# Performance work log

Hardware: AMD Instinct MI355X
Metric: run time of the kernel (lower is better)

The kernel has to match this reference:

```python
import jax, jax.numpy as jnp
import numpy as np

B, S, D = 2, 2048, 1024
H = 16
HD = D // H  # 64
SCALE = HD ** -0.5


def setup_inputs() -> dict:
    key = jax.random.key(0)
    ks = jax.random.split(key, 9)
    init = lambda k, shape: jax.random.normal(k, shape, dtype=jnp.float32) * (1.0 / np.sqrt(shape[-1]))
    return {
        "x": jax.random.normal(ks[0], (B, S, D), dtype=jnp.float32),
        "wq": init(ks[1], (D, D)), "bq": jnp.zeros((D,), jnp.float32),
        "wk": init(ks[2], (D, D)), "bk": jnp.zeros((D,), jnp.float32),
        "wv": init(ks[3], (D, D)), "bv": jnp.zeros((D,), jnp.float32),
        "wo": init(ks[4], (D, D)), "bo": jnp.zeros((D,), jnp.float32),
    }


def reference(x, wq, bq, wk, bk, wv, bv, wo, bo):
    b, s, d = x.shape
    # projections -> [b, h, s, hd]
    q = (x @ wq + bq).reshape(b, s, H, HD).transpose(0, 2, 1, 3)
    k = (x @ wk + bk).reshape(b, s, H, HD).transpose(0, 2, 1, 3)
    v = (x @ wv + bv).reshape(b, s, H, HD).transpose(0, 2, 1, 3)
    # full causal attention (chunked loop in original computes exactly this)
    scores = jnp.einsum("bhqd,bhkd->bhqk", q, k) * SCALE
    causal = jnp.tril(jnp.ones((s, s), dtype=bool))
    scores = jnp.where(causal, scores, -jnp.inf)
    weights = jax.nn.softmax(scores, axis=-1)
    out = jnp.einsum("bhqk,bhkd->bhqd", weights, v)
    out = out.transpose(0, 2, 1, 3).reshape(b, s, d)
    return out @ wo + bo
```

## Files before the change

kernel.cpp:

```cpp
#include <hip/hip_runtime.h>
#include <hip/hip_bf16.h>
#include <cstdint>

#define B_  2
#define S_  2048
#define D_  1024
#define H_  16
#define HD_ 64
#define M_  (B_ * S_)
static constexpr float SC_LOG2E = 0.125f * 1.44269504088896f;

typedef __bf16 bf16x8 __attribute__((ext_vector_type(8)));
typedef __bf16 bf16x4 __attribute__((ext_vector_type(4)));
typedef float  f32x4  __attribute__((ext_vector_type(4)));

__device__ __forceinline__ unsigned short f2b(float f) {
  union { float f; unsigned u; } x; x.f = f;
  unsigned r = x.u + 0x7FFF + ((x.u >> 16) & 1);
  return (unsigned short)(r >> 16);
}

__device__ __forceinline__ void gl_lds16(const unsigned short* g, unsigned short* l) {
  __builtin_amdgcn_global_load_lds((const __attribute__((address_space(1))) void*)g,
                                   (__attribute__((address_space(3))) void*)l, 16, 0, 0);
}

__device__ __forceinline__ void bar_lgkm() {
  asm volatile("s_waitcnt lgkmcnt(0)\n\ts_barrier" ::: "memory");
}
__device__ __forceinline__ void bar_vm2() {
  asm volatile("s_waitcnt vmcnt(2) lgkmcnt(0)\n\ts_barrier" ::: "memory");
}
__device__ __forceinline__ void bar_vm0() {
  asm volatile("s_waitcnt vmcnt(0) lgkmcnt(0)\n\ts_barrier" ::: "memory");
}

__global__ void cvt_all_kernel(const float* __restrict__ x,
                               const float* __restrict__ w0, const float* __restrict__ w1,
                               const float* __restrict__ w2, const float* __restrict__ w3,
                               unsigned short* __restrict__ xb,
                               unsigned short* __restrict__ o0, unsigned short* __restrict__ o1,
                               unsigned short* __restrict__ o2, unsigned short* __restrict__ o3) {
  int tx = threadIdx.x, ty = threadIdx.y;
  if (blockIdx.z == 4) {
    int tid = ty * 32 + tx;
    int base = ((int)blockIdx.y * 32 + (int)blockIdx.x) * 1024 + tid;
    const float4* xf = (const float4*)x;
    ushort4* ob = (ushort4*)xb;
#pragma unroll
    for (int j = 0; j < 4; j++) {
      float4 v = xf[base + j * 256];
      ushort4 r;
      r.x = f2b(v.x); r.y = f2b(v.y); r.z = f2b(v.z); r.w = f2b(v.w);
      ob[base + j * 256] = r;
    }
    return;
  }
  const float* w = blockIdx.z == 0 ? w0 : blockIdx.z == 1 ? w1 : blockIdx.z == 2 ? w2 : w3;
  unsigned short* o = blockIdx.z == 0 ? o0 : blockIdx.z == 1 ? o1 : blockIdx.z == 2 ? o2 : o3;
  __shared__ float t[32][33];
  int x0 = blockIdx.x * 32, y0 = blockIdx.y * 32;
#pragma unroll
  for (int j = 0; j < 4; j++)
    t[ty + j * 8][tx] = w[(size_t)(y0 + ty + j * 8) * D_ + x0 + tx];
  __syncthreads();
#pragma unroll
  for (int j = 0; j < 4; j++)
    o[(size_t)(x0 + ty + j * 8) * D_ + y0 + tx] = f2b(t[tx][ty + j * 8]);
}

__global__ __launch_bounds__(512) void qkv_gemm_kernel(
    const unsigned short* __restrict__ xb,
    const unsigned short* __restrict__ wqt, const unsigned short* __restrict__ wkt,
    const unsigned short* __restrict__ wvt,
    const float* __restrict__ bq, const float* __restrict__ bk, const float* __restrict__ bv,
    unsigned short* __restrict__ qo, unsigned short* __restrict__ ko, unsigned short* __restrict__ vo) {
  const unsigned short* wt = blockIdx.z == 0 ? wqt : blockIdx.z == 1 ? wkt : wvt;
  const float* bias        = blockIdx.z == 0 ? bq  : blockIdx.z == 1 ? bk  : bv;
  unsigned short* out      = blockIdx.z == 0 ? qo  : blockIdx.z == 1 ? ko  : vo;
  const float scl = blockIdx.z == 0 ? SC_LOG2E : 1.0f;

  __shared__ __align__(16) unsigned short smem[6 * 4096];
  const int tid = threadIdx.x;
  const int lane = tid & 63, wid = tid >> 6;
  const int wm = wid & 1, wn = wid >> 1;
  const int m0 = blockIdx.x * 128, n0 = blockIdx.y * 128;
  const int l15 = lane & 15, q4 = lane >> 4;
  const int srow = tid >> 2, skc = (tid & 3) * 8;

  f32x4 zero = {0.f, 0.f, 0.f, 0.f};
  f32x4 acc[4][2];
#pragma unroll
  for (int mt = 0; mt < 4; mt++)
#pragma unroll
    for (int nt = 0; nt < 2; nt++) acc[mt][nt] = zero;

  const unsigned short* ap = xb + (size_t)(m0 + srow) * D_ + skc;
  const unsigned short* bp = wt + (size_t)(n0 + srow) * D_ + skc;
  gl_lds16(ap,      smem + tid * 8);
  gl_lds16(bp,      smem + 12288 + tid * 8);
  gl_lds16(ap + 32, smem + 4096 + tid * 8);
  gl_lds16(bp + 32, smem + 12288 + 4096 + tid * 8);

  int bc = 0;
  for (int it = 0; it < 32; it++) {
    if (it < 31) bar_vm2(); else bar_vm0();
    if (it + 2 < 32) {
      int bn_ = bc < 1 ? bc + 2 : bc - 1;
      gl_lds16(ap + (it + 2) * 32, smem + bn_ * 4096 + tid * 8);
      gl_lds16(bp + (it + 2) * 32, smem + 12288 + bn_ * 4096 + tid * 8);
    }
    const unsigned short* Ab = smem + bc * 4096;
    const unsigned short* Bb = smem + 12288 + bc * 4096;
    bf16x8 af[4], bfv[2];
#pragma unroll
    for (int mt = 0; mt < 4; mt++) af[mt]  = *(const bf16x8*)(Ab + (wm * 64 + mt * 16 + l15) * 32 + q4 * 8);
#pragma unroll
    for (int nt = 0; nt < 2; nt++) bfv[nt] = *(const bf16x8*)(Bb + (wn * 32 + nt * 16 + l15) * 32 + q4 * 8);
#pragma unroll
    for (int mt = 0; mt < 4; mt++)
#pragma unroll
      for (int nt = 0; nt < 2; nt++)
        acc[mt][nt] = __builtin_amdgcn_mfma_f32_16x16x32_bf16(af[mt], bfv[nt], acc[mt][nt], 0, 0, 0);
    bc = bc == 2 ? 0 : bc + 1;
  }

  if (blockIdx.z < 2) {
#pragma unroll
    for (int nt = 0; nt < 2; nt++) {
      int n = n0 + wn * 32 + nt * 16 + l15;
      float bn = bias[n];
      int h = n >> 6, hd = n & 63;
#pragma unroll
      for (int mt = 0; mt < 4; mt++) {
#pragma unroll
        for (int r = 0; r < 4; r++) {
          int m = m0 + wm * 64 + mt * 16 + q4 * 4 + r;
          int b = m >> 11, s = m & (S_ - 1);
          out[(((size_t)(b * H_ + h)) * S_ + s) * HD_ + hd] = f2b((acc[mt][nt][r] + bn) * scl);
        }
      }
    }
  } else {
    unsigned short* buf = smem;
#pragma unroll
    for (int p = 0; p < 2; p++) {
      __syncthreads();
      if ((wn >> 1) == p) {
#pragma unroll
        for (int nt = 0; nt < 2; nt++) {
          int np = (wn & 1) * 32 + nt * 16 + l15;
          float bn = bias[n0 + p * 64 + np];
#pragma unroll
          for (int mt = 0; mt < 4; mt++) {
            f32x4 vb = acc[mt][nt];
            vb[0] += bn; vb[1] += bn; vb[2] += bn; vb[3] += bn;
            bf16x4 pk = __builtin_convertvector(vb, bf16x4);
            *(bf16x4*)(&buf[np * 136 + wm * 64 + mt * 16 + q4 * 4]) = pk;
          }
        }
      }
      __syncthreads();
#pragma unroll
      for (int i = 0; i < 2; i++) {
        int ci = tid + i * 512;
        int np = ci >> 4, c = ci & 15;
        int n = n0 + p * 64 + np;
        int h = n >> 6, hd = n & 63;
        int m = m0 + c * 8;
        int b = m >> 11, s = m & (S_ - 1);
        *(uint4*)(out + (((size_t)(b * H_ + h)) * HD_ + hd) * S_ + s) = *(const uint4*)(buf + np * 136 + c * 8);
      }
    }
  }
}

__global__ __launch_bounds__(512, 4) void attn_kernel(
    const unsigned short* __restrict__ Q, const unsigned short* __restrict__ K,
    const unsigned short* __restrict__ Vt_g, unsigned short* __restrict__ O) {
  const int id = blockIdx.x;
  const int u = id >> 8, v = id & 255;
  const int bh = v & 31;
  const int t = v >> 5;
  const int qi = u ? (15 - t) : t;
  const int b = bh >> 4, h = bh & 15;
  const unsigned short* Qh = Q    + (size_t)bh * S_ * HD_;
  const unsigned short* Kh = K    + (size_t)bh * S_ * HD_;
  const unsigned short* Vh = Vt_g + (size_t)bh * HD_ * S_;

  __shared__ __align__(16) unsigned short Ks[2][64 * 64];
  __shared__ __align__(16) unsigned short Vt[2][64 * 64];
  __shared__ __align__(16) unsigned short Ps[8][16 * 72];

  const int tid = threadIdx.x, lane = tid & 63, w = tid >> 6;
  const int l15 = lane & 15, q4 = lane >> 4;
  const int kx = (l15 & 7) << 3;
  const int kcA = (q4 * 8) ^ kx, kcB = (q4 * 8 + 32) ^ kx;
  const int vc0 = (q4 * 8) ^ kx, vc1 = (32 + q4 * 8) ^ kx;
  unsigned short* Pw = &Ps[w][0];

  const int srow = tid >> 3;
  const int scolS = (((tid & 7) ^ (srow & 7)) * 8);
  const unsigned short* kg = Kh + (size_t)srow * HD_ + (tid & 7) * 8;
  const unsigned short* vg = Vh + (size_t)srow * S_  + (tid & 7) * 8;

  const int q0 = qi * 128;
  const int nkt = 2 * qi + 2;
  const int qlo = q0 + w * 16;
  const int qmax = qlo + 15;
  const int qrow = qlo + l15;

  const unsigned short* qp = Qh + (size_t)qrow * HD_ + q4 * 8;
  bf16x8 bq0 = *(const bf16x8*)(qp);
  bf16x8 bq1 = *(const bf16x8*)(qp + 32);

  float m_i = -1e30f, l_i = 0.f;
  f32x4 zero = {0.f, 0.f, 0.f, 0.f};
  f32x4 o_acc[4];
#pragma unroll
  for (int t4 = 0; t4 < 4; t4++) o_acc[t4] = zero;

  uint4 kp = *(const uint4*)(kg);
  uint4 vp = *(const uint4*)(vg);

  for (int kt = 0; kt < nkt; kt++) {
    const int k0 = kt * 64;
    unsigned short* Kb = Ks[kt & 1];
    unsigned short* Vb = Vt[kt & 1];
    *(uint4*)(Kb + srow * 64 + scolS) = kp;
    *(uint4*)(Vb + srow * 64 + scolS) = vp;
    bar_lgkm();
    if (kt + 1 < nkt) {
      kp = *(const uint4*)(kg + (size_t)(kt + 1) * 64 * HD_);
      vp = *(const uint4*)(vg + (kt + 1) * 64);
    }

    if (k0 <= qmax) {
      f32x4 sc[4];
#pragma unroll
      for (int nt = 0; nt < 4; nt++) sc[nt] = zero;
      __builtin_amdgcn_s_setprio(1);
#pragma unroll
      for (int nt = 0; nt < 4; nt++) {
        bf16x8 ak0 = *(const bf16x8*)(Kb + (nt * 16 + l15) * 64 + kcA);
        bf16x8 ak1 = *(const bf16x8*)(Kb + (nt * 16 + l15) * 64 + kcB);
        sc[nt] = __builtin_amdgcn_mfma_f32_16x16x32_bf16(ak0, bq0, sc[nt], 0, 0, 0);
        sc[nt] = __builtin_amdgcn_mfma_f32_16x16x32_bf16(ak1, bq1, sc[nt], 0, 0, 0);
      }
      __builtin_amdgcn_s_setprio(0);

      if ((k0 + 63) > qlo) {
#pragma unroll
        for (int nt = 0; nt < 4; nt++)
#pragma unroll
          for (int r = 0; r < 4; r++) {
            int key = k0 + nt * 16 + q4 * 4 + r;
            if (key > qrow) sc[nt][r] = -1e30f;
          }
      }

      float am[4];
#pragma unroll
      for (int nt = 0; nt < 4; nt++)
        am[nt] = fmaxf(fmaxf(sc[nt][0], sc[nt][1]), fmaxf(sc[nt][2], sc[nt][3]));
      am[0] = fmaxf(am[0], am[2]); am[1] = fmaxf(am[1], am[3]);
      float mx = fmaxf(am[0], am[1]);
      mx = fmaxf(mx, __shfl_xor(mx, 16));
      mx = fmaxf(mx, __shfl_xor(mx, 32));
      mx = fmaxf(mx, m_i);

      if (!__all(mx - m_i <= 10.0f)) {
        float alpha = __builtin_amdgcn_exp2f(m_i - mx);
        m_i = mx;
        l_i *= alpha;
#pragma unroll
        for (int r = 0; r < 4; r++) {
          float ar = __shfl(alpha, q4 * 4 + r);
          o_acc[0][r] *= ar; o_acc[1][r] *= ar; o_acc[2][r] *= ar; o_acc[3][r] *= ar;
        }
      }

      float sm[4];
#pragma unroll
      for (int nt = 0; nt < 4; nt++) {
        f32x4 pv;
#pragma unroll
        for (int r = 0; r < 4; r++) pv[r] = __builtin_amdgcn_exp2f(sc[nt][r] - m_i);
        sc[nt] = pv;
        sm[nt] = (pv[0] + pv[1]) + (pv[2] + pv[3]);
      }
      float rs = (sm[0] + sm[2]) + (sm[1] + sm[3]);
      rs += __shfl_xor(rs, 16);
      rs += __shfl_xor(rs, 32);
      l_i += rs;

#pragma unroll
      for (int nt = 0; nt < 4; nt++) {
        bf16x4 pk = __builtin_convertvector(sc[nt], bf16x4);
        *(bf16x4*)(Pw + l15 * 72 + nt * 16 + q4 * 4) = pk;
      }
      __threadfence_block();
      bf16x8 ap0 = *(const bf16x8*)(Pw + l15 * 72 + q4 * 8);
      bf16x8 ap1 = *(const bf16x8*)(Pw + l15 * 72 + 32 + q4 * 8);
      __builtin_amdgcn_s_setprio(1);
#pragma unroll
      for (int nt2 = 0; nt2 < 4; nt2++) {
        bf16x8 bv0 = *(const bf16x8*)(Vb + (nt2 * 16 + l15) * 64 + vc0);
        o_acc[nt2] = __builtin_amdgcn_mfma_f32_16x16x32_bf16(ap0, bv0, o_acc[nt2], 0, 0, 0);
      }
#pragma unroll
      for (int nt2 = 0; nt2 < 4; nt2++) {
        bf16x8 bv1 = *(const bf16x8*)(Vb + (nt2 * 16 + l15) * 64 + vc1);
        o_acc[nt2] = __builtin_amdgcn_mfma_f32_16x16x32_bf16(ap1, bv1, o_acc[nt2], 0, 0, 0);
      }
      __builtin_amdgcn_s_setprio(0);
    }
  }

#pragma unroll
  for (int r = 0; r < 4; r++) {
    float lr = __shfl(l_i, q4 * 4 + r);
    float inv = 1.0f / lr;
    int s_ = q0 + w * 16 + q4 * 4 + r;
#pragma unroll
    for (int nt2 = 0; nt2 < 4; nt2++)
      O[((size_t)(b * S_ + s_)) * D_ + h * HD_ + nt2 * 16 + l15] = f2b(o_acc[nt2][r] * inv);
  }
}

__global__ __launch_bounds__(512) void out_gemm_kernel(
    const unsigned short* __restrict__ ab, const unsigned short* __restrict__ wot,
    const float* __restrict__ bo, float* __restrict__ out) {
  __shared__ __align__(16) unsigned short smem[6 * 4096];
  const int tid = threadIdx.x;
  const int lane = tid & 63, wid = tid >> 6;
  const int wm = wid & 1, wn = wid >> 1;
  const int m0 = blockIdx.x * 128, n0 = blockIdx.y * 128;
  const int l15 = lane & 15, q4 = lane >> 4;
  const int srow = tid >> 2, skc = (tid & 3) * 8;

  f32x4 zero = {0.f, 0.f, 0.f, 0.f};
  f32x4 acc[4][2];
#pragma unroll
  for (int mt = 0; mt < 4; mt++)
#pragma unroll
    for (int nt = 0; nt < 2; nt++) acc[mt][nt] = zero;

  const unsigned short* ap = ab  + (size_t)(m0 + srow) * D_ + skc;
  const unsigned short* bp = wot + (size_t)(n0 + srow) * D_ + skc;
  gl_lds16(ap,      smem + tid * 8);
  gl_lds16(bp,      smem + 12288 + tid * 8);
  gl_lds16(ap + 32, smem + 4096 + tid * 8);
  gl_lds16(bp + 32, smem + 12288 + 4096 + tid * 8);

  int bc = 0;
  for (int it = 0; it < 32; it++) {
    if (it < 31) bar_vm2(); else bar_vm0();
    if (it + 2 < 32) {
      int bn_ = bc < 1 ? bc + 2 : bc - 1;
      gl_lds16(ap + (it + 2) * 32, smem + bn_ * 4096 + tid * 8);
      gl_lds16(bp + (it + 2) * 32, smem + 12288 + bn_ * 4096 + tid * 8);
    }
    const unsigned short* Ab = smem + bc * 4096;
    const unsigned short* Bb = smem + 12288 + bc * 4096;
    bf16x8 af[4], bfv[2];
#pragma unroll
    for (int mt = 0; mt < 4; mt++) af[mt]  = *(const bf16x8*)(Ab + (wm * 64 + mt * 16 + l15) * 32 + q4 * 8);
#pragma unroll
    for (int nt = 0; nt < 2; nt++) bfv[nt] = *(const bf16x8*)(Bb + (wn * 32 + nt * 16 + l15) * 32 + q4 * 8);
#pragma unroll
    for (int mt = 0; mt < 4; mt++)
#pragma unroll
      for (int nt = 0; nt < 2; nt++)
        acc[mt][nt] = __builtin_amdgcn_mfma_f32_16x16x32_bf16(af[mt], bfv[nt], acc[mt][nt], 0, 0, 0);
    bc = bc == 2 ? 0 : bc + 1;
  }

#pragma unroll
  for (int nt = 0; nt < 2; nt++) {
    int n = n0 + wn * 32 + nt * 16 + l15;
    float bn = bo[n];
#pragma unroll
    for (int mt = 0; mt < 4; mt++) {
#pragma unroll
      for (int r = 0; r < 4; r++) {
        int m = m0 + wm * 64 + mt * 16 + q4 * 4 + r;
        out[(size_t)m * D_ + n] = acc[mt][nt][r] + bn;
      }
    }
  }
}

extern "C" void kernel_launch(void* const* d_in, const int* in_sizes, int n_in,
                              void* d_out, int out_size, void* d_ws, size_t ws_size,
                              hipStream_t stream) {
  const float* x  = (const float*)d_in[0];
  const float* wq = (const float*)d_in[1];
  const float* bq = (const float*)d_in[2];
  const float* wk = (const float*)d_in[3];
  const float* bk = (const float*)d_in[4];
  const float* wv = (const float*)d_in[5];
  const float* bv = (const float*)d_in[6];
  const float* wo = (const float*)d_in[7];
  const float* bo = (const float*)d_in[8];
  float* out = (float*)d_out;

  char* ws = (char*)d_ws;
  unsigned short* xb  = (unsigned short*)(ws);
  unsigned short* wqt = (unsigned short*)(ws + (8u  << 20));
  unsigned short* wkt = (unsigned short*)(ws + (10u << 20));
  unsigned short* wvt = (unsigned short*)(ws + (12u << 20));
  unsigned short* wot = (unsigned short*)(ws + (14u << 20));
  unsigned short* qb  = (unsigned short*)(ws + (16u << 20));
  unsigned short* kb  = (unsigned short*)(ws + (24u << 20));
  unsigned short* vtg = (unsigned short*)(ws + (32u << 20));
  unsigned short* ab  = xb;

  cvt_all_kernel<<<dim3(32, 32, 5), dim3(32, 8), 0, stream>>>(x, wq, wk, wv, wo, xb, wqt, wkt, wvt, wot);
  qkv_gemm_kernel<<<dim3(32, 8, 3), dim3(512), 0, stream>>>(xb, wqt, wkt, wvt, bq, bk, bv, qb, kb, vtg);
  attn_kernel<<<dim3(512), dim3(512), 0, stream>>>(qb, kb, vtg, ab);
  out_gemm_kernel<<<dim3(32, 8), dim3(512), 0, stream>>>(ab, wot, bo, out);
}
```

Measured before the change: 181.7 us.

## Restructure attention onto 32x32x16 MFMA with register P and direct-to-LDS loads

The attention kernel now runs 4 waves per block, each owning 32 query rows, and uses 32x32x16 bf16 MFMAs in place of 16x16x32. The P matrix is packed to bf16 with v_cvt_pk and rearranged with permlane32_swap, so it stays in registers instead of going through LDS. K and V tiles are loaded with global_load_lds double buffering instead of register staging, and the output is staged through LDS so the global stores are coalesced 16-byte writes. The goal is to cut LDS traffic and instruction overhead per MFMA. In exchange the kernel holds larger accumulator vectors, which may raise register pressure and lower occupancy.

```diff
diff --git a/kernel.cpp b/kernel.cpp
--- a/kernel.cpp
+++ b/kernel.cpp
@@ -13,11 +13,22 @@
 typedef __bf16 bf16x8 __attribute__((ext_vector_type(8)));
 typedef __bf16 bf16x4 __attribute__((ext_vector_type(4)));
 typedef float  f32x4  __attribute__((ext_vector_type(4)));
+typedef float  f32x16 __attribute__((ext_vector_type(16)));
+typedef unsigned u32x2 __attribute__((ext_vector_type(2)));
 
 __device__ __forceinline__ unsigned short f2b(float f) {
   union { float f; unsigned u; } x; x.f = f;
   unsigned r = x.u + 0x7FFF + ((x.u >> 16) & 1);
   return (unsigned short)(r >> 16);
+}
+
+__device__ __forceinline__ unsigned cvtpk(float lo, float hi) {
+  unsigned r;
+  asm("v_cvt_pk_bf16_f32 %0, %1, %2" : "=v"(r) : "v"(lo), "v"(hi));
+  return r;
+}
+__device__ __forceinline__ u32x2 pswap(unsigned a, unsigned b) {
+  return __builtin_amdgcn_permlane32_swap(a, b, false, false);
 }
 
 __device__ __forceinline__ void gl_lds16(const unsigned short* g, unsigned short* l) {
@@ -175,14 +186,13 @@
   }
 }
 
-__global__ __launch_bounds__(512, 4) void attn_kernel(
+__global__ __launch_bounds__(256, 2) void attn_kernel(
     const unsigned short* __restrict__ Q, const unsigned short* __restrict__ K,
     const unsigned short* __restrict__ Vt_g, unsigned short* __restrict__ O) {
   const int id = blockIdx.x;
-  const int u = id >> 8, v = id & 255;
-  const int bh = v & 31;
-  const int t = v >> 5;
-  const int qi = u ? (15 - t) : t;
+  const int bh = id & 31;
+  const int t = id >> 5;
+  const int qi = (t < 8) ? (15 - t) : (t - 8);
   const int b = bh >> 4, h = bh & 15;
   const unsigned short* Qh = Q    + (size_t)bh * S_ * HD_;
   const unsigned short* Kh = K    + (size_t)bh * S_ * HD_;
@@ -190,141 +200,159 @@
 
   __shared__ __align__(16) unsigned short Ks[2][64 * 64];
   __shared__ __align__(16) unsigned short Vt[2][64 * 64];
-  __shared__ __align__(16) unsigned short Ps[8][16 * 72];
+  __shared__ __align__(16) unsigned short Sw[4][32 * 72];
 
   const int tid = threadIdx.x, lane = tid & 63, w = tid >> 6;
-  const int l15 = lane & 15, q4 = lane >> 4;
-  const int kx = (l15 & 7) << 3;
-  const int kcA = (q4 * 8) ^ kx, kcB = (q4 * 8 + 32) ^ kx;
-  const int vc0 = (q4 * 8) ^ kx, vc1 = (32 + q4 * 8) ^ kx;
-  unsigned short* Pw = &Ps[w][0];
-
-  const int srow = tid >> 3;
-  const int scolS = (((tid & 7) ^ (srow & 7)) * 8);
-  const unsigned short* kg = Kh + (size_t)srow * HD_ + (tid & 7) * 8;
-  const unsigned short* vg = Vh + (size_t)srow * S_  + (tid & 7) * 8;
-
-  const int q0 = qi * 128;
-  const int nkt = 2 * qi + 2;
-  const int qlo = q0 + w * 16;
-  const int qmax = qlo + 15;
-  const int qrow = qlo + l15;
-
-  const unsigned short* qp = Qh + (size_t)qrow * HD_ + q4 * 8;
-  bf16x8 bq0 = *(const bf16x8*)(qp);
-  bf16x8 bq1 = *(const bf16x8*)(qp + 32);
+  const int myk = lane & 31, hi5 = lane >> 5;
+  const int q0 = qi * 128, nkt = 2 * qi + 2;
+  const int qlo = q0 + w * 32, qmax = qlo + 31;
+  const int qrow = qlo + myk;
+
+  int kso[2], vso[2];
+#pragma unroll
+  for (int j = 0; j < 2; j++) {
+    int c = tid + j * 256, row = c >> 3, c8 = c & 7;
+    int sc_ = (c8 ^ (row & 7)) * 8;
+    kso[j] = row * HD_ + sc_;
+    vso[j] = row * S_ + sc_;
+  }
+
+  bf16x8 qf[4];
+#pragma unroll
+  for (int kk = 0; kk < 4; kk++)
+    qf[kk] = *(const bf16x8*)(Qh + (size_t)qrow * HD_ + kk * 16 + hi5 * 8);
+
+#pragma unroll
+  for (int j = 0; j < 2; j++) {
+    gl_lds16(Kh + kso[j], &Ks[0][0] + (tid + j * 256) * 8);
+    gl_lds16(Vh + vso[j], &Vt[0][0] + (tid + j * 256) * 8);
+  }
 
   float m_i = -1e30f, l_i = 0.f;
-  f32x4 zero = {0.f, 0.f, 0.f, 0.f};
-  f32x4 o_acc[4];
-#pragma unroll
-  for (int t4 = 0; t4 < 4; t4++) o_acc[t4] = zero;
-
-  uint4 kp = *(const uint4*)(kg);
-  uint4 vp = *(const uint4*)(vg);
+  f32x16 oa0, oa1;
+#pragma unroll
+  for (int i = 0; i < 16; i++) { oa0[i] = 0.f; oa1[i] = 0.f; }
 
   for (int kt = 0; kt < nkt; kt++) {
     const int k0 = kt * 64;
-    unsigned short* Kb = Ks[kt & 1];
-    unsigned short* Vb = Vt[kt & 1];
-    *(uint4*)(Kb + srow * 64 + scolS) = kp;
-    *(uint4*)(Vb + srow * 64 + scolS) = vp;
-    bar_lgkm();
+    bar_vm0();
     if (kt + 1 < nkt) {
-      kp = *(const uint4*)(kg + (size_t)(kt + 1) * 64 * HD_);
-      vp = *(const uint4*)(vg + (kt + 1) * 64);
-    }
-
-    if (k0 <= qmax) {
-      f32x4 sc[4];
-#pragma unroll
-      for (int nt = 0; nt < 4; nt++) sc[nt] = zero;
-      __builtin_amdgcn_s_setprio(1);
-#pragma unroll
-      for (int nt = 0; nt < 4; nt++) {
-        bf16x8 ak0 = *(const bf16x8*)(Kb + (nt * 16 + l15) * 64 + kcA);
-        bf16x8 ak1 = *(const bf16x8*)(Kb + (nt * 16 + l15) * 64 + kcB);
-        sc[nt] = __builtin_amdgcn_mfma_f32_16x16x32_bf16(ak0, bq0, sc[nt], 0, 0, 0);
-        sc[nt] = __builtin_amdgcn_mfma_f32_16x16x32_bf16(ak1, bq1, sc[nt], 0, 0, 0);
-      }
-      __builtin_amdgcn_s_setprio(0);
-
-      if ((k0 + 63) > qlo) {
-#pragma unroll
-        for (int nt = 0; nt < 4; nt++)
-#pragma unroll
-          for (int r = 0; r < 4; r++) {
-            int key = k0 + nt * 16 + q4 * 4 + r;
-            if (key > qrow) sc[nt][r] = -1e30f;
-          }
-      }
-
-      float am[4];
-#pragma unroll
-      for (int nt = 0; nt < 4; nt++)
-        am[nt] = fmaxf(fmaxf(sc[nt][0], sc[nt][1]), fmaxf(sc[nt][2], sc[nt][3]));
-      am[0] = fmaxf(am[0], am[2]); am[1] = fmaxf(am[1], am[3]);
-      float mx = fmaxf(am[0], am[1]);
-      mx = fmaxf(mx, __shfl_xor(mx, 16));
-      mx = fmaxf(mx, __shfl_xor(mx, 32));
-      mx = fmaxf(mx, m_i);
-
-      if (!__all(mx - m_i <= 10.0f)) {
-        float alpha = __builtin_amdgcn_exp2f(m_i - mx);
-        m_i = mx;
-        l_i *= alpha;
-#pragma unroll
-        for (int r = 0; r < 4; r++) {
-          float ar = __shfl(alpha, q4 * 4 + r);
-          o_acc[0][r] *= ar; o_acc[1][r] *= ar; o_acc[2][r] *= ar; o_acc[3][r] *= ar;
-        }
-      }
-
-      float sm[4];
-#pragma unroll
-      for (int nt = 0; nt < 4; nt++) {
-        f32x4 pv;
-#pragma unroll
-        for (int r = 0; r < 4; r++) pv[r] = __builtin_amdgcn_exp2f(sc[nt][r] - m_i);
-        sc[nt] = pv;
-        sm[nt] = (pv[0] + pv[1]) + (pv[2] + pv[3]);
-      }
-      float rs = (sm[0] + sm[2]) + (sm[1] + sm[3]);
-      rs += __shfl_xor(rs, 16);
-      rs += __shfl_xor(rs, 32);
-      l_i += rs;
-
-#pragma unroll
-      for (int nt = 0; nt < 4; nt++) {
-        bf16x4 pk = __builtin_convertvector(sc[nt], bf16x4);
-        *(bf16x4*)(Pw + l15 * 72 + nt * 16 + q4 * 4) = pk;
-      }
-      __threadfence_block();
-      bf16x8 ap0 = *(const bf16x8*)(Pw + l15 * 72 + q4 * 8);
-      bf16x8 ap1 = *(const bf16x8*)(Pw + l15 * 72 + 32 + q4 * 8);
-      __builtin_amdgcn_s_setprio(1);
-#pragma unroll
-      for (int nt2 = 0; nt2 < 4; nt2++) {
-        bf16x8 bv0 = *(const bf16x8*)(Vb + (nt2 * 16 + l15) * 64 + vc0);
-        o_acc[nt2] = __builtin_amdgcn_mfma_f32_16x16x32_bf16(ap0, bv0, o_acc[nt2], 0, 0, 0);
-      }
-#pragma unroll
-      for (int nt2 = 0; nt2 < 4; nt2++) {
-        bf16x8 bv1 = *(const bf16x8*)(Vb + (nt2 * 16 + l15) * 64 + vc1);
-        o_acc[nt2] = __builtin_amdgcn_mfma_f32_16x16x32_bf16(ap1, bv1, o_acc[nt2], 0, 0, 0);
-      }
-      __builtin_amdgcn_s_setprio(0);
-    }
-  }
-
-#pragma unroll
-  for (int r = 0; r < 4; r++) {
-    float lr = __shfl(l_i, q4 * 4 + r);
-    float inv = 1.0f / lr;
-    int s_ = q0 + w * 16 + q4 * 4 + r;
-#pragma unroll
-    for (int nt2 = 0; nt2 < 4; nt2++)
-      O[((size_t)(b * S_ + s_)) * D_ + h * HD_ + nt2 * 16 + l15] = f2b(o_acc[nt2][r] * inv);
+      unsigned short* Kd = &Ks[(kt + 1) & 1][0];
+      unsigned short* Vd = &Vt[(kt + 1) & 1][0];
+#pragma unroll
+      for (int j = 0; j < 2; j++) {
+        gl_lds16(Kh + (kt + 1) * 64 * HD_ + kso[j], Kd + (tid + j * 256) * 8);
+        gl_lds16(Vh + (kt + 1) * 64 + vso[j],       Vd + (tid + j * 256) * 8);
+      }
+    }
+    if (k0 > qmax) continue;
+
+    const unsigned short* Kb = &Ks[kt & 1][0];
+    const unsigned short* Vb = &Vt[kt & 1][0];
+
+    f32x16 sc0, sc1;
+#pragma unroll
+    for (int i = 0; i < 16; i++) { sc0[i] = 0.f; sc1[i] = 0.f; }
+    __builtin_amdgcn_s_setprio(1);
+#pragma unroll
+    for (int kk = 0; kk < 4; kk++) {
+      const int off = ((kk * 2 + hi5) ^ (myk & 7)) * 8;
+      bf16x8 a0 = *(const bf16x8*)(Kb + myk * 64 + off);
+      bf16x8 a1 = *(const bf16x8*)(Kb + (32 + myk) * 64 + off);
+      sc0 = __builtin_amdgcn_mfma_f32_32x32x16_bf16(a0, qf[kk], sc0, 0, 0, 0);
+      sc1 = __builtin_amdgcn_mfma_f32_32x32x16_bf16(a1, qf[kk], sc1, 0, 0, 0);
+    }
+    __builtin_amdgcn_s_setprio(0);
+
+    if (k0 + 63 > qlo) {
+#pragma unroll
+      for (int rg = 0; rg < 16; rg++) {
+        const int r = (rg & 3) + 8 * (rg >> 2) + 4 * hi5;
+        if (k0 + r > qrow)      sc0[rg] = -1e30f;
+        if (k0 + 32 + r > qrow) sc1[rg] = -1e30f;
+      }
+    }
+
+    float am[8];
+#pragma unroll
+    for (int i = 0; i < 8; i++)
+      am[i] = fmaxf(fmaxf(sc0[i], sc0[i + 8]), fmaxf(sc1[i], sc1[i + 8]));
+#pragma unroll
+    for (int sr = 4; sr > 0; sr >>= 1)
+#pragma unroll
+      for (int i = 0; i < sr; i++) am[i] = fmaxf(am[i], am[i + sr]);
+    float mx = fmaxf(am[0], __shfl_xor(am[0], 32));
+    mx = fmaxf(mx, m_i);
+
+    if (!__all(mx - m_i <= 10.0f)) {
+      float alpha = __builtin_amdgcn_exp2f(m_i - mx);
+      m_i = mx;
+      l_i *= alpha;
+#pragma unroll
+      for (int i = 0; i < 16; i++) { oa0[i] *= alpha; oa1[i] *= alpha; }
+    }
+
+#pragma unroll
+    for (int i = 0; i < 16; i++) sc0[i] = __builtin_amdgcn_exp2f(sc0[i] - m_i);
+#pragma unroll
+    for (int i = 0; i < 16; i++) sc1[i] = __builtin_amdgcn_exp2f(sc1[i] - m_i);
+    float sm[8];
+#pragma unroll
+    for (int i = 0; i < 8; i++) sm[i] = (sc0[i] + sc0[i + 8]) + (sc1[i] + sc1[i + 8]);
+#pragma unroll
+    for (int sr = 4; sr > 0; sr >>= 1)
+#pragma unroll
+      for (int i = 0; i < sr; i++) sm[i] += sm[i + sr];
+    l_i += sm[0] + __shfl_xor(sm[0], 32);
+
+    unsigned wa[8], wb[8];
+#pragma unroll
+    for (int i = 0; i < 8; i++) {
+      wa[i] = cvtpk(sc0[2 * i], sc0[2 * i + 1]);
+      wb[i] = cvtpk(sc1[2 * i], sc1[2 * i + 1]);
+    }
+    union { unsigned u[4]; bf16x8 v; } pf0, pf1, pf2, pf3;
+    { u32x2 s0 = pswap(wa[0], wa[2]), s1 = pswap(wa[1], wa[3]);
+      pf0.u[0] = s0[0]; pf0.u[1] = s1[0]; pf0.u[2] = s0[1]; pf0.u[3] = s1[1]; }
+    { u32x2 s0 = pswap(wa[4], wa[6]), s1 = pswap(wa[5], wa[7]);
+      pf1.u[0] = s0[0]; pf1.u[1] = s1[0]; pf1.u[2] = s0[1]; pf1.u[3] = s1[1]; }
+    { u32x2 s0 = pswap(wb[0], wb[2]), s1 = pswap(wb[1], wb[3]);
+      pf2.u[0] = s0[0]; pf2.u[1] = s1[0]; pf2.u[2] = s0[1]; pf2.u[3] = s1[1]; }
+    { u32x2 s0 = pswap(wb[4], wb[6]), s1 = pswap(wb[5], wb[7]);
+      pf3.u[0] = s0[0]; pf3.u[1] = s1[0]; pf3.u[2] = s0[1]; pf3.u[3] = s1[1]; }
+
+    __builtin_amdgcn_s_setprio(1);
+#pragma unroll
+    for (int ks = 0; ks < 4; ks++) {
+      const int off = ((ks * 2 + hi5) ^ (myk & 7)) * 8;
+      bf16x8 v0 = *(const bf16x8*)(Vb + myk * 64 + off);
+      bf16x8 v1 = *(const bf16x8*)(Vb + (32 + myk) * 64 + off);
+      bf16x8 pk = ks == 0 ? pf0.v : ks == 1 ? pf1.v : ks == 2 ? pf2.v : pf3.v;
+      oa0 = __builtin_amdgcn_mfma_f32_32x32x16_bf16(v0, pk, oa0, 0, 0, 0);
+      oa1 = __builtin_amdgcn_mfma_f32_32x32x16_bf16(v1, pk, oa1, 0, 0, 0);
+    }
+    __builtin_amdgcn_s_setprio(0);
+  }
+
+  const float inv = 1.0f / l_i;
+#pragma unroll
+  for (int i = 0; i < 16; i++) { oa0[i] *= inv; oa1[i] *= inv; }
+  unsigned short* sw = &Sw[w][0];
+#pragma unroll
+  for (int g = 0; g < 4; g++) {
+    u32x2 d0, d1;
+    d0[0] = cvtpk(oa0[4 * g], oa0[4 * g + 1]);
+    d0[1] = cvtpk(oa0[4 * g + 2], oa0[4 * g + 3]);
+    d1[0] = cvtpk(oa1[4 * g], oa1[4 * g + 1]);
+    d1[1] = cvtpk(oa1[4 * g + 2], oa1[4 * g + 3]);
+    *(u32x2*)(sw + myk * 72 + g * 8 + 4 * hi5)      = d0;
+    *(u32x2*)(sw + myk * 72 + 32 + g * 8 + 4 * hi5) = d1;
+  }
+#pragma unroll
+  for (int rr = 0; rr < 4; rr++) {
+    int qq = rr * 8 + (lane >> 3);
+    uint4 d = *(const uint4*)(sw + qq * 72 + (lane & 7) * 8);
+    *(uint4*)(O + ((size_t)(b * S_ + qlo + qq)) * D_ + h * 64 + (lane & 7) * 8) = d;
   }
 }
 
@@ -418,6 +446,6 @@
 
   cvt_all_kernel<<<dim3(32, 32, 5), dim3(32, 8), 0, stream>>>(x, wq, wk, wv, wo, xb, wqt, wkt, wvt, wot);
   qkv_gemm_kernel<<<dim3(32, 8, 3), dim3(512), 0, stream>>>(xb, wqt, wkt, wvt, bq, bk, bv, qb, kb, vtg);
-  attn_kernel<<<dim3(512), dim3(512), 0, stream>>>(qb, kb, vtg, ab);
+  attn_kernel<<<dim3(512), dim3(256), 0, stream>>>(qb, kb, vtg, ab);
   out_gemm_kernel<<<dim3(32, 8), dim3(512), 0, stream>>>(ab, wot, bo, out);
 }
```

Measured after the change: 188.1 us. 1.03x slower.

## Drop LDS staging of K/V in attention and shrink query tiles to 64 rows

Applied to the files above, without the earlier changes.

The attention kernel now reads K and V fragments straight from global memory (relying on L1/L2) instead of double-buffering them through shared memory with a barrier each iteration. Blocks shrink to 256 threads covering 64 query rows, and the grid doubles to 1024 with a four-way reversed tile ordering to balance causal work. This removes the per-tile barriers and LDS traffic and raises block count, but it trades that for redundant global/cache loads, since each wave fetches K/V independently with less coalesced access.

```diff
diff --git a/kernel.cpp b/kernel.cpp
--- a/kernel.cpp
+++ b/kernel.cpp
@@ -175,39 +175,28 @@
   }
 }
 
-__global__ __launch_bounds__(512, 4) void attn_kernel(
+__global__ __launch_bounds__(256, 4) void attn_kernel(
     const unsigned short* __restrict__ Q, const unsigned short* __restrict__ K,
     const unsigned short* __restrict__ Vt_g, unsigned short* __restrict__ O) {
   const int id = blockIdx.x;
-  const int u = id >> 8, v = id & 255;
-  const int bh = v & 31;
-  const int t = v >> 5;
-  const int qi = u ? (15 - t) : t;
+  const int bh = id & 31;
+  const int tIdx = id >> 5;
+  const int u = tIdx >> 3, t8 = tIdx & 7;
+  const int qi = (u == 0) ? t8 : (u == 1) ? (15 - t8) : (u == 2) ? (16 + t8) : (31 - t8);
   const int b = bh >> 4, h = bh & 15;
   const unsigned short* Qh = Q    + (size_t)bh * S_ * HD_;
   const unsigned short* Kh = K    + (size_t)bh * S_ * HD_;
   const unsigned short* Vh = Vt_g + (size_t)bh * HD_ * S_;
 
-  __shared__ __align__(16) unsigned short Ks[2][64 * 64];
-  __shared__ __align__(16) unsigned short Vt[2][64 * 64];
-  __shared__ __align__(16) unsigned short Ps[8][16 * 72];
+  __shared__ __align__(16) unsigned short Ps[4][16 * 72];
 
   const int tid = threadIdx.x, lane = tid & 63, w = tid >> 6;
   const int l15 = lane & 15, q4 = lane >> 4;
-  const int kx = (l15 & 7) << 3;
-  const int kcA = (q4 * 8) ^ kx, kcB = (q4 * 8 + 32) ^ kx;
-  const int vc0 = (q4 * 8) ^ kx, vc1 = (32 + q4 * 8) ^ kx;
   unsigned short* Pw = &Ps[w][0];
 
-  const int srow = tid >> 3;
-  const int scolS = (((tid & 7) ^ (srow & 7)) * 8);
-  const unsigned short* kg = Kh + (size_t)srow * HD_ + (tid & 7) * 8;
-  const unsigned short* vg = Vh + (size_t)srow * S_  + (tid & 7) * 8;
-
-  const int q0 = qi * 128;
-  const int nkt = 2 * qi + 2;
+  const int q0 = qi * 64;
+  const int nkt = qi + 1;
   const int qlo = q0 + w * 16;
-  const int qmax = qlo + 15;
   const int qrow = qlo + l15;
 
   const unsigned short* qp = Qh + (size_t)qrow * HD_ + q4 * 8;
@@ -220,101 +209,88 @@
 #pragma unroll
   for (int t4 = 0; t4 < 4; t4++) o_acc[t4] = zero;
 
-  uint4 kp = *(const uint4*)(kg);
-  uint4 vp = *(const uint4*)(vg);
-
   for (int kt = 0; kt < nkt; kt++) {
     const int k0 = kt * 64;
-    unsigned short* Kb = Ks[kt & 1];
-    unsigned short* Vb = Vt[kt & 1];
-    *(uint4*)(Kb + srow * 64 + scolS) = kp;
-    *(uint4*)(Vb + srow * 64 + scolS) = vp;
-    bar_lgkm();
-    if (kt + 1 < nkt) {
-      kp = *(const uint4*)(kg + (size_t)(kt + 1) * 64 * HD_);
-      vp = *(const uint4*)(vg + (kt + 1) * 64);
-    }
-
-    if (k0 <= qmax) {
-      f32x4 sc[4];
-#pragma unroll
-      for (int nt = 0; nt < 4; nt++) sc[nt] = zero;
-      __builtin_amdgcn_s_setprio(1);
-#pragma unroll
-      for (int nt = 0; nt < 4; nt++) {
-        bf16x8 ak0 = *(const bf16x8*)(Kb + (nt * 16 + l15) * 64 + kcA);
-        bf16x8 ak1 = *(const bf16x8*)(Kb + (nt * 16 + l15) * 64 + kcB);
-        sc[nt] = __builtin_amdgcn_mfma_f32_16x16x32_bf16(ak0, bq0, sc[nt], 0, 0, 0);
-        sc[nt] = __builtin_amdgcn_mfma_f32_16x16x32_bf16(ak1, bq1, sc[nt], 0, 0, 0);
-      }
-      __builtin_amdgcn_s_setprio(0);
-
-      if ((k0 + 63) > qlo) {
-#pragma unroll
-        for (int nt = 0; nt < 4; nt++)
-#pragma unroll
-          for (int r = 0; r < 4; r++) {
-            int key = k0 + nt * 16 + q4 * 4 + r;
-            if (key > qrow) sc[nt][r] = -1e30f;
-          }
-      }
-
-      float am[4];
+
+    f32x4 sc[4];
+#pragma unroll
+    for (int nt = 0; nt < 4; nt++) sc[nt] = zero;
+    __builtin_amdgcn_s_setprio(1);
+#pragma unroll
+    for (int nt = 0; nt < 4; nt++) {
+      const unsigned short* kr = Kh + (size_t)(k0 + nt * 16 + l15) * HD_ + q4 * 8;
+      bf16x8 ak0 = *(const bf16x8*)(kr);
+      bf16x8 ak1 = *(const bf16x8*)(kr + 32);
+      sc[nt] = __builtin_amdgcn_mfma_f32_16x16x32_bf16(ak0, bq0, sc[nt], 0, 0, 0);
+      sc[nt] = __builtin_amdgcn_mfma_f32_16x16x32_bf16(ak1, bq1, sc[nt], 0, 0, 0);
+    }
+    __builtin_amdgcn_s_setprio(0);
+
+    if (k0 + 63 > qlo) {
 #pragma unroll
       for (int nt = 0; nt < 4; nt++)
-        am[nt] = fmaxf(fmaxf(sc[nt][0], sc[nt][1]), fmaxf(sc[nt][2], sc[nt][3]));
-      am[0] = fmaxf(am[0], am[2]); am[1] = fmaxf(am[1], am[3]);
-      float mx = fmaxf(am[0], am[1]);
-      mx = fmaxf(mx, __shfl_xor(mx, 16));
-      mx = fmaxf(mx, __shfl_xor(mx, 32));
-      mx = fmaxf(mx, m_i);
-
-      if (!__all(mx - m_i <= 10.0f)) {
-        float alpha = __builtin_amdgcn_exp2f(m_i - mx);
-        m_i = mx;
-        l_i *= alpha;
 #pragma unroll
         for (int r = 0; r < 4; r++) {
-          float ar = __shfl(alpha, q4 * 4 + r);
-          o_acc[0][r] *= ar; o_acc[1][r] *= ar; o_acc[2][r] *= ar; o_acc[3][r] *= ar;
+          int key = k0 + nt * 16 + q4 * 4 + r;
+          if (key > qrow) sc[nt][r] = -1e30f;
         }
-      }
-
-      float sm[4];
-#pragma unroll
-      for (int nt = 0; nt < 4; nt++) {
-        f32x4 pv;
-#pragma unroll
-        for (int r = 0; r < 4; r++) pv[r] = __builtin_amdgcn_exp2f(sc[nt][r] - m_i);
-        sc[nt] = pv;
-        sm[nt] = (pv[0] + pv[1]) + (pv[2] + pv[3]);
-      }
-      float rs = (sm[0] + sm[2]) + (sm[1] + sm[3]);
-      rs += __shfl_xor(rs, 16);
-      rs += __shfl_xor(rs, 32);
-      l_i += rs;
-
-#pragma unroll
-      for (int nt = 0; nt < 4; nt++) {
-        bf16x4 pk = __builtin_convertvector(sc[nt], bf16x4);
-        *(bf16x4*)(Pw + l15 * 72 + nt * 16 + q4 * 4) = pk;
-      }
-      __threadfence_block();
-      bf16x8 ap0 = *(const bf16x8*)(Pw + l15 * 72 + q4 * 8);
-      bf16x8 ap1 = *(const bf16x8*)(Pw + l15 * 72 + 32 + q4 * 8);
-      __builtin_amdgcn_s_setprio(1);
-#pragma unroll
-      for (int nt2 = 0; nt2 < 4; nt2++) {
-        bf16x8 bv0 = *(const bf16x8*)(Vb + (nt2 * 16 + l15) * 64 + vc0);
-        o_acc[nt2] = __builtin_amdgcn_mfma_f32_16x16x32_bf16(ap0, bv0, o_acc[nt2], 0, 0, 0);
-      }
-#pragma unroll
-      for (int nt2 = 0; nt2 < 4; nt2++) {
-        bf16x8 bv1 = *(const bf16x8*)(Vb + (nt2 * 16 + l15) * 64 + vc1);
-        o_acc[nt2] = __builtin_amdgcn_mfma_f32_16x16x32_bf16(ap1, bv1, o_acc[nt2], 0, 0, 0);
-      }
-      __builtin_amdgcn_s_setprio(0);
-    }
+    }
+
+    float am[4];
+#pragma unroll
+    for (int nt = 0; nt < 4; nt++)
+      am[nt] = fmaxf(fmaxf(sc[nt][0], sc[nt][1]), fmaxf(sc[nt][2], sc[nt][3]));
+    am[0] = fmaxf(am[0], am[2]); am[1] = fmaxf(am[1], am[3]);
+    float mx = fmaxf(am[0], am[1]);
+    mx = fmaxf(mx, __shfl_xor(mx, 16));
+    mx = fmaxf(mx, __shfl_xor(mx, 32));
+    mx = fmaxf(mx, m_i);
+
+    if (!__all(mx - m_i <= 10.0f)) {
+      float alpha = __builtin_amdgcn_exp2f(m_i - mx);
+      m_i = mx;
+      l_i *= alpha;
+#pragma unroll
+      for (int r = 0; r < 4; r++) {
+        float ar = __shfl(alpha, q4 * 4 + r);
+        o_acc[0][r] *= ar; o_acc[1][r] *= ar; o_acc[2][r] *= ar; o_acc[3][r] *= ar;
+      }
+    }
+
+    float sm[4];
+#pragma unroll
+    for (int nt = 0; nt < 4; nt++) {
+      f32x4 pv;
+#pragma unroll
+      for (int r = 0; r < 4; r++) pv[r] = __builtin_amdgcn_exp2f(sc[nt][r] - m_i);
+      sc[nt] = pv;
+      sm[nt] = (pv[0] + pv[1]) + (pv[2] + pv[3]);
+    }
+    float rs = (sm[0] + sm[2]) + (sm[1] + sm[3]);
+    rs += __shfl_xor(rs, 16);
+    rs += __shfl_xor(rs, 32);
+    l_i += rs;
+
+#pragma unroll
+    for (int nt = 0; nt < 4; nt++) {
+      bf16x4 pk = __builtin_convertvector(sc[nt], bf16x4);
+      *(bf16x4*)(Pw + l15 * 72 + nt * 16 + q4 * 4) = pk;
+    }
+    __threadfence_block();
+    bf16x8 ap0 = *(const bf16x8*)(Pw + l15 * 72 + q4 * 8);
+    bf16x8 ap1 = *(const bf16x8*)(Pw + l15 * 72 + 32 + q4 * 8);
+    __builtin_amdgcn_s_setprio(1);
+#pragma unroll
+    for (int nt2 = 0; nt2 < 4; nt2++) {
+      bf16x8 bv0 = *(const bf16x8*)(Vh + (size_t)(nt2 * 16 + l15) * S_ + k0 + q4 * 8);
+      o_acc[nt2] = __builtin_amdgcn_mfma_f32_16x16x32_bf16(ap0, bv0, o_acc[nt2], 0, 0, 0);
+    }
+#pragma unroll
+    for (int nt2 = 0; nt2 < 4; nt2++) {
+      bf16x8 bv1 = *(const bf16x8*)(Vh + (size_t)(nt2 * 16 + l15) * S_ + k0 + 32 + q4 * 8);
+      o_acc[nt2] = __builtin_amdgcn_mfma_f32_16x16x32_bf16(ap1, bv1, o_acc[nt2], 0, 0, 0);
+    }
+    __builtin_amdgcn_s_setprio(0);
   }
 
 #pragma unroll
@@ -418,6 +394,6 @@
 
   cvt_all_kernel<<<dim3(32, 32, 5), dim3(32, 8), 0, stream>>>(x, wq, wk, wv, wo, xb, wqt, wkt, wvt, wot);
   qkv_gemm_kernel<<<dim3(32, 8, 3), dim3(512), 0, stream>>>(xb, wqt, wkt, wvt, bq, bk, bv, qb, kb, vtg);
-  attn_kernel<<<dim3(512), dim3(512), 0, stream>>>(qb, kb, vtg, ab);
+  attn_kernel<<<dim3(1024), dim3(256), 0, stream>>>(qb, kb, vtg, ab);
   out_gemm_kernel<<<dim3(32, 8), dim3(512), 0, stream>>>(ab, wot, bo, out);
 }
```

Result: slower. 261.0 us (+43.6%).

## Load V fragments directly from global into registers, drop V LDS staging

Applied to the files above, without the earlier changes.

The attention kernel stops staging V^T tiles through shared memory. Each wave now loads its V MFMA operands straight from global memory per active key tile. This removes the V LDS stores and reads and halves LDS use, which may raise occupancy. In exchange every wave redundantly fetches the same V tile and global latency lands directly before the PV MFMAs with no software prefetch. The block-to-query-tile mapping also changes so that heavy (late) query tiles are dispatched first.

```diff
diff --git a/kernel.cpp b/kernel.cpp
--- a/kernel.cpp
+++ b/kernel.cpp
@@ -179,30 +179,26 @@
     const unsigned short* __restrict__ Q, const unsigned short* __restrict__ K,
     const unsigned short* __restrict__ Vt_g, unsigned short* __restrict__ O) {
   const int id = blockIdx.x;
-  const int u = id >> 8, v = id & 255;
-  const int bh = v & 31;
-  const int t = v >> 5;
-  const int qi = u ? (15 - t) : t;
+  const int bh = id & 31;
+  const int t = id >> 5;
+  const int qi = (t < 8) ? (15 - t) : (t - 8);
   const int b = bh >> 4, h = bh & 15;
   const unsigned short* Qh = Q    + (size_t)bh * S_ * HD_;
   const unsigned short* Kh = K    + (size_t)bh * S_ * HD_;
   const unsigned short* Vh = Vt_g + (size_t)bh * HD_ * S_;
 
   __shared__ __align__(16) unsigned short Ks[2][64 * 64];
-  __shared__ __align__(16) unsigned short Vt[2][64 * 64];
   __shared__ __align__(16) unsigned short Ps[8][16 * 72];
 
   const int tid = threadIdx.x, lane = tid & 63, w = tid >> 6;
   const int l15 = lane & 15, q4 = lane >> 4;
   const int kx = (l15 & 7) << 3;
   const int kcA = (q4 * 8) ^ kx, kcB = (q4 * 8 + 32) ^ kx;
-  const int vc0 = (q4 * 8) ^ kx, vc1 = (32 + q4 * 8) ^ kx;
   unsigned short* Pw = &Ps[w][0];
 
   const int srow = tid >> 3;
   const int scolS = (((tid & 7) ^ (srow & 7)) * 8);
   const unsigned short* kg = Kh + (size_t)srow * HD_ + (tid & 7) * 8;
-  const unsigned short* vg = Vh + (size_t)srow * S_  + (tid & 7) * 8;
 
   const int q0 = qi * 128;
   const int nkt = 2 * qi + 2;
@@ -221,21 +217,24 @@
   for (int t4 = 0; t4 < 4; t4++) o_acc[t4] = zero;
 
   uint4 kp = *(const uint4*)(kg);
-  uint4 vp = *(const uint4*)(vg);
 
   for (int kt = 0; kt < nkt; kt++) {
     const int k0 = kt * 64;
     unsigned short* Kb = Ks[kt & 1];
-    unsigned short* Vb = Vt[kt & 1];
     *(uint4*)(Kb + srow * 64 + scolS) = kp;
-    *(uint4*)(Vb + srow * 64 + scolS) = vp;
     bar_lgkm();
-    if (kt + 1 < nkt) {
+    if (kt + 1 < nkt)
       kp = *(const uint4*)(kg + (size_t)(kt + 1) * 64 * HD_);
-      vp = *(const uint4*)(vg + (kt + 1) * 64);
-    }
 
     if (k0 <= qmax) {
+      bf16x8 vfa[4], vfb[4];
+#pragma unroll
+      for (int nt2 = 0; nt2 < 4; nt2++) {
+        const unsigned short* vr = Vh + (size_t)(nt2 * 16 + l15) * S_ + k0 + q4 * 8;
+        vfa[nt2] = *(const bf16x8*)(vr);
+        vfb[nt2] = *(const bf16x8*)(vr + 32);
+      }
+
       f32x4 sc[4];
 #pragma unroll
       for (int nt = 0; nt < 4; nt++) sc[nt] = zero;
@@ -304,15 +303,11 @@
       bf16x8 ap1 = *(const bf16x8*)(Pw + l15 * 72 + 32 + q4 * 8);
       __builtin_amdgcn_s_setprio(1);
 #pragma unroll
-      for (int nt2 = 0; nt2 < 4; nt2++) {
-        bf16x8 bv0 = *(const bf16x8*)(Vb + (nt2 * 16 + l15) * 64 + vc0);
-        o_acc[nt2] = __builtin_amdgcn_mfma_f32_16x16x32_bf16(ap0, bv0, o_acc[nt2], 0, 0, 0);
-      }
-#pragma unroll
-      for (int nt2 = 0; nt2 < 4; nt2++) {
-        bf16x8 bv1 = *(const bf16x8*)(Vb + (nt2 * 16 + l15) * 64 + vc1);
-        o_acc[nt2] = __builtin_amdgcn_mfma_f32_16x16x32_bf16(ap1, bv1, o_acc[nt2], 0, 0, 0);
-      }
+      for (int nt2 = 0; nt2 < 4; nt2++)
+        o_acc[nt2] = __builtin_amdgcn_mfma_f32_16x16x32_bf16(ap0, vfa[nt2], o_acc[nt2], 0, 0, 0);
+#pragma unroll
+      for (int nt2 = 0; nt2 < 4; nt2++)
+        o_acc[nt2] = __builtin_amdgcn_mfma_f32_16x16x32_bf16(ap1, vfb[nt2], o_acc[nt2], 0, 0, 0);
       __builtin_amdgcn_s_setprio(0);
     }
   }
```

After: 211.5 us. 16.4% more time.
